# Kernel optimization log

Measured on AMD Instinct MI355X. Metric: run time of the kernel, lower is better.

Reference implementation:

```python
import jax, jax.numpy as jnp
import numpy as np

B, T, H, K = 64, 512, 768, 32


def setup_inputs() -> dict:
    key = jax.random.key(0)
    ks = jax.random.split(key, 6)
    x = jax.random.normal(ks[0], (B, T, H), jnp.float32)
    y = jax.random.randint(ks[1], (B, T), 0, K)
    sequence_lengths = jax.random.randint(ks[2], (B,), 1, T + 1)
    W = jax.random.normal(ks[3], (H, K), jnp.float32) * 0.02
    b = jnp.zeros((K,), jnp.float32)
    transition_params = jax.random.normal(ks[4], (K, K), jnp.float32) * 0.1
    return dict(x=x, y=y, sequence_lengths=sequence_lengths, W=W, b=b,
                transition_params=transition_params)


def _crf_log_norm(pot, lengths, trans):
    # pot: [B,T,K]; forward algorithm with per-example length masking
    alpha0 = pot[:, 0]
    def step(alpha, inp):
        pot_t, t = inp
        new = jax.nn.logsumexp(alpha[:, :, None] + trans[None], axis=1) + pot_t
        keep = (t < lengths)[:, None]
        return jnp.where(keep, new, alpha), None
    xs = (jnp.swapaxes(pot[:, 1:], 0, 1), jnp.arange(1, pot.shape[1]))
    alpha, _ = jax.lax.scan(step, alpha0, xs)
    return jax.nn.logsumexp(alpha, axis=-1)  # [B]


def _crf_sequence_score(pot, y, lengths, trans):
    t_idx = jnp.arange(pot.shape[1])
    mask_u = (t_idx[None, :] < lengths[:, None]).astype(pot.dtype)      # [B,T]
    unary = jnp.take_along_axis(pot, y[..., None], axis=2)[..., 0]      # [B,T]
    unary = jnp.sum(unary * mask_u, axis=1)
    mask_b = (t_idx[None, :-1] < (lengths - 1)[:, None]).astype(pot.dtype)
    binary = trans[y[:, :-1], y[:, 1:]]                                 # [B,T-1]
    binary = jnp.sum(binary * mask_b, axis=1)
    return unary + binary


def _crf_decode(pot, lengths, trans):
    Bb, Tt, Kk = pot.shape
    alpha0 = pot[:, 0]
    ident = jnp.broadcast_to(jnp.arange(Kk), (Bb, Kk))
    def fwd(alpha, inp):
        pot_t, t = inp
        scores = alpha[:, :, None] + trans[None]   # [B,K,K] prev->cur
        bp = jnp.argmax(scores, axis=1)            # [B,K]
        new = jnp.max(scores, axis=1) + pot_t
        keep = (t < lengths)[:, None]
        alpha = jnp.where(keep, new, alpha)
        bp = jnp.where(keep, bp, ident)            # identity past end of seq
        return alpha, bp
    xs = (jnp.swapaxes(pot[:, 1:], 0, 1), jnp.arange(1, Tt))
    alpha, bps = jax.lax.scan(fwd, alpha0, xs)     # bps: [T-1,B,K]
    last = jnp.argmax(alpha, axis=-1)              # [B]
    def back(tag, bp):
        prev = jnp.take_along_axis(bp, tag[:, None], axis=1)[:, 0]
        return prev, prev
    _, prevs = jax.lax.scan(back, last, bps, reverse=True)  # [T-1,B]
    tags = jnp.concatenate([prevs, last[None]], axis=0).T   # [B,T]
    return tags


def reference(x, y, sequence_lengths, W, b, transition_params):
    pot = jnp.einsum('bth,hk->btk', x, W) + b      # dense projection to tag space
    log_likelihood = (_crf_sequence_score(pot, y, sequence_lengths, transition_params)
                      - _crf_log_norm(pot, sequence_lengths, transition_params))
    preds = _crf_decode(pot, sequence_lengths, transition_params)
    mask = (jnp.arange(pot.shape[1])[None, :] < sequence_lengths[:, None]).astype(preds.dtype)
    preds = preds * mask
    return log_likelihood, preds
```

## Files before the change

kernel.cpp:

```cpp
#include <hip/hip_runtime.h>
#include <hip/hip_bf16.h>
#include <stdint.h>


#define TT 512
#define KK 32
#define HH 768
#define NB 64

#define WS_POT 0
#define WS_VA  4198400
#define WS_BP  8396800
#define WS_LOGZ 9445376
#define WS_LAST 9445632

template <int CTRL>
__device__ __forceinline__ float dppx(float x) {
  return __int_as_float(__builtin_amdgcn_update_dpp(
      0, __float_as_int(x), CTRL, 0xF, 0xF, true));
}

__device__ __forceinline__ float xor16f(float x) {
  float d = x, s = x;
  asm volatile("v_permlane16_swap_b32 %0, %1" : "+v"(d), "+v"(s));
  return __uint_as_float(__float_as_uint(d) ^ __float_as_uint(s) ^ __float_as_uint(x));
}
__device__ __forceinline__ float xor32f(float x) {
  float d = x, s = x;
  asm volatile("v_permlane32_swap_b32 %0, %1" : "+v"(d), "+v"(s));
  return __uint_as_float(__float_as_uint(d) ^ __float_as_uint(s) ^ __float_as_uint(x));
}

__device__ __forceinline__ float redmax32(float v) {
  v = fmaxf(v, dppx<0xB1>(v));
  v = fmaxf(v, dppx<0x4E>(v));
  v = fmaxf(v, dppx<0x141>(v));
  v = fmaxf(v, dppx<0x128>(v));
  v = fmaxf(v, xor16f(v));
  return v;
}
__device__ __forceinline__ float redsum32(float v) {
  v += dppx<0xB1>(v);
  v += dppx<0x4E>(v);
  v += dppx<0x141>(v);
  v += dppx<0x128>(v);
  v += xor16f(v);
  return v;
}

__device__ __forceinline__ int gmap(int m) {
  return ((m & 1) ? 1 : 0) ^ ((m & 2) ? 2 : 0) ^ ((m & 4) ? 7 : 0) ^ ((m & 8) ? 8 : 0);
}

#define REPL_TREE(A)                                            \
  A[1] = dppx<0xB1>(A[0]);                                      \
  _Pragma("unroll") for (int p = 0; p < 2; ++p) A[2 + p] = dppx<0x4E>(A[p]);  \
  _Pragma("unroll") for (int p = 0; p < 4; ++p) A[4 + p] = dppx<0x141>(A[p]); \
  _Pragma("unroll") for (int p = 0; p < 8; ++p) A[8 + p] = dppx<0x128>(A[p]);

__global__ __launch_bounds__(256) void gemm_pot(const float* __restrict__ x,
                                                const float* __restrict__ W,
                                                const float* __restrict__ bias,
                                                float* __restrict__ pot) {
  __shared__ float4 xs4[64][16];
  __shared__ float4 wt4[32][16];
  const int tid = threadIdx.x;
  const int row0 = blockIdx.x * 64;
  const int cg = tid & 15;
  const int rg = tid >> 4;
  const int c0 = cg * 2;
  float acc[4][2] = {{0.f, 0.f}, {0.f, 0.f}, {0.f, 0.f}, {0.f, 0.f}};

  for (int h0 = 0; h0 < HH; h0 += 64) {
#pragma unroll
    for (int p = 0; p < 4; ++p) {
      const int fi = tid + p * 256;
      const int r = fi >> 4, s = fi & 15;
      const float4 v = *(const float4*)(&x[(size_t)(row0 + r) * HH + h0 + s * 4]);
      xs4[r][s ^ ((r >> 2) & 3)] = v;
    }
    {
      const int c = tid & 31;
      const int hb = (tid >> 5) * 8;
      float* wf = (float*)(&wt4[0][0]);
#pragma unroll
      for (int i2 = 0; i2 < 8; ++i2) {
        const int hh = hb + i2;
        const int slot = (hh >> 2) ^ ((c >> 1) & 15);
        wf[c * 64 + slot * 4 + (hh & 3)] = W[(size_t)(h0 + hh) * KK + c];
      }
    }
    __syncthreads();
#pragma unroll
    for (int s = 0; s < 16; ++s) {
      float4 xv[4];
#pragma unroll
      for (int i = 0; i < 4; ++i) xv[i] = xs4[rg * 4 + i][s ^ (rg & 3)];
      const float4 wv0 = wt4[c0][s ^ cg];
      const float4 wv1 = wt4[c0 + 1][s ^ cg];
#pragma unroll
      for (int i = 0; i < 4; ++i) {
        acc[i][0] += xv[i].x * wv0.x + xv[i].y * wv0.y + xv[i].z * wv0.z + xv[i].w * wv0.w;
        acc[i][1] += xv[i].x * wv1.x + xv[i].y * wv1.y + xv[i].z * wv1.z + xv[i].w * wv1.w;
      }
    }
    __syncthreads();
  }
#pragma unroll
  for (int i = 0; i < 4; ++i) {
    const int row = row0 + rg * 4 + i;
    float2 o = make_float2(acc[i][0] + bias[c0], acc[i][1] + bias[c0 + 1]);
    *(float2*)(&pot[(size_t)row * KK + c0]) = o;
  }
}

__global__ __launch_bounds__(64) void scan2(const float* __restrict__ pot,
                                            const int* __restrict__ lens,
                                            const float* __restrict__ trans,
                                            float* __restrict__ va,
                                            float* __restrict__ logZ,
                                            int* __restrict__ last) {
  const int lane = threadIdx.x;
  const int k = lane & 31;
  const int jh = lane >> 5;
  const bool is_lse = (blockIdx.x < 64);
  const int b = is_lse ? blockIdx.x : blockIdx.x - 64;
  const int len = lens[b];
  const float* pp = pot + (size_t)b * (TT * KK) + k;

  if (is_lse) {
    float etrx[16];
#pragma unroll
    for (int m = 0; m < 16; ++m)
      etrx[m] = __expf(trans[((k ^ gmap(m) ^ (jh << 4)) << 5) + k]);
    const float a0 = pp[0];
    const float M0 = redmax32(a0);
    float a = __expf(a0 - M0);
    float alog = M0;
    float ep[8], en[8];
#pragma unroll
    for (int i = 0; i < 8; ++i) ep[i] = __expf(pp[(size_t)(1 + i) * KK]);
    for (int tb = 1; tb < len; tb += 8) {
#pragma unroll
      for (int i = 0; i < 8; ++i) en[i] = pp[(size_t)(tb + 8 + i) * KK];
#pragma unroll
      for (int i = 0; i < 8; ++i) {
        const int t = tb + i;
        if (t >= len) break;
        float A[16];
        const float u16 = xor16f(a);
        A[0] = jh ? u16 : a;
        REPL_TREE(A)
        float d0 = 0.f, d1 = 0.f, d2 = 0.f, d3 = 0.f;
#pragma unroll
        for (int p = 0; p < 4; ++p) {
          d0 += A[4 * p + 0] * etrx[4 * p + 0];
          d1 += A[4 * p + 1] * etrx[4 * p + 1];
          d2 += A[4 * p + 2] * etrx[4 * p + 2];
          d3 += A[4 * p + 3] * etrx[4 * p + 3];
        }
        float part = (d0 + d1) + (d2 + d3);
        a = (part + xor32f(part)) * ep[i];
        if ((t & 7) == 0) {
          const float mx = redmax32(a);
          alog += __logf(mx);
          a *= __builtin_amdgcn_rcpf(mx);
        }
      }
#pragma unroll
      for (int i = 0; i < 8; ++i) ep[i] = __expf(en[i]);
    }
    const float ssum = redsum32(a);
    if (lane == 0) logZ[b] = alog + __logf(ssum);
  } else {
    float trx[16];
#pragma unroll
    for (int m = 0; m < 16; ++m)
      trx[m] = trans[((k ^ gmap(m) ^ (jh << 4)) << 5) + k];
    float a = pp[0];
    float* vap = va + (size_t)b * (TT * KK) + k;
    if (lane < 32) vap[0] = a;
    float pb[8], pn[8];
#pragma unroll
    for (int i = 0; i < 8; ++i) pb[i] = pp[(size_t)(1 + i) * KK];
    for (int tb = 1; tb < len; tb += 8) {
#pragma unroll
      for (int i = 0; i < 8; ++i) pn[i] = pp[(size_t)(tb + 8 + i) * KK];
#pragma unroll
      for (int i = 0; i < 8; ++i) {
        const int t = tb + i;
        if (t >= len) break;
        float A[16];
        const float u16 = xor16f(a);
        A[0] = jh ? u16 : a;
        REPL_TREE(A)
        float s_[16];
#pragma unroll
        for (int m = 0; m < 16; ++m) s_[m] = A[m] + trx[m];
        const float m0 = fmaxf(fmaxf(s_[0], s_[1]), fmaxf(s_[2], s_[3]));
        const float m1 = fmaxf(fmaxf(s_[4], s_[5]), fmaxf(s_[6], s_[7]));
        const float m2 = fmaxf(fmaxf(s_[8], s_[9]), fmaxf(s_[10], s_[11]));
        const float m3 = fmaxf(fmaxf(s_[12], s_[13]), fmaxf(s_[14], s_[15]));
        const float part = fmaxf(fmaxf(m0, m1), fmaxf(m2, m3));
        a = fmaxf(part, xor32f(part)) + pb[i];
        if (lane < 32) vap[(size_t)t * KK] = a;
      }
#pragma unroll
      for (int i = 0; i < 8; ++i) pb[i] = pn[i];
    }
    float v = a;
    int idx = k;
#pragma unroll
    for (int mm = 16; mm >= 1; mm >>= 1) {
      const float vo = __shfl_xor(v, mm, 32);
      const int io = __shfl_xor(idx, mm, 32);
      if (vo > v || (vo == v && io < idx)) { v = vo; idx = io; }
    }
    if (lane == 0) last[b] = idx;
  }
}

__global__ __launch_bounds__(256) void bp_extract(const float* __restrict__ va,
                                                  const float* __restrict__ trans,
                                                  unsigned char* __restrict__ bp) {
  const int b = blockIdx.x >> 3;
  const int tbase = (blockIdx.x & 7) * 64;
  const int k = threadIdx.x & 31;
  const int ts = threadIdx.x >> 5;
  float tr[32];
#pragma unroll
  for (int j = 0; j < 32; ++j) tr[j] = trans[j * KK + k];
#pragma unroll
  for (int it = 0; it < 8; ++it) {
    const int t = tbase + it * 8 + ts;
    if (t < 1) continue;
    const float* row = va + ((size_t)b * TT + (t - 1)) * KK;
    float best = row[0] + tr[0];
    int bi = 0;
#pragma unroll
    for (int j = 1; j < 32; ++j) {
      const float s = row[j] + tr[j];
      if (s > best) { best = s; bi = j; }
    }
    bp[((size_t)b * TT + t) * KK + k] = (unsigned char)bi;
  }
}

__global__ __launch_bounds__(256) void backtrace_kernel(
    const unsigned char* __restrict__ bp, const int* __restrict__ lens,
    const int* __restrict__ last, const float* __restrict__ pot,
    const int* __restrict__ y, const float* __restrict__ trans,
    const float* __restrict__ logZ, float* __restrict__ out) {
  __shared__ unsigned char Ls[32736];
  __shared__ unsigned char sA[512], sB[512];
  __shared__ float red[256];
  const int b = blockIdx.x, tid = threadIdx.x;
  const int len = lens[b];

  for (int i = tid; i < TT * KK; i += 256) {
    const int t = i >> 5, k = i & 31;
    Ls[i] = (t >= 1 && t < len) ? bp[((size_t)b * TT + t) * KK + k] : (unsigned char)k;
  }
  __syncthreads();

  int off_prev = 0, cnt = 512;
  for (int l = 1; l <= 9; ++l) {
    const int off = 32 * (1024 - (1024 >> l));
    const int n = cnt >> 1;
    for (int i = tid; i < n * 32; i += 256) {
      const int m = i >> 5, k = i & 31;
      const int inner = Ls[off_prev + (2 * m + 1) * 32 + k];
      Ls[off + i] = Ls[off_prev + (2 * m) * 32 + inner];
    }
    __syncthreads();
    off_prev = off;
    cnt = n;
  }

  if (tid == 0) sA[0] = (unsigned char)last[b];
  __syncthreads();

  unsigned char* cur = sA;
  unsigned char* nxt = sB;
  int c2 = 1;
  for (int l = 9; l >= 1; --l) {
    const int offm = 32 * (1024 - (1024 >> (l - 1)));
    for (int i = tid; i < c2; i += 256) {
      const unsigned char s = cur[i];
      nxt[2 * i + 1] = s;
      nxt[2 * i] = Ls[offm + (2 * i + 1) * 32 + s];
    }
    __syncthreads();
    unsigned char* tmp = cur; cur = nxt; nxt = tmp;
    c2 <<= 1;
  }

  for (int t = tid; t < TT; t += 256)
    out[NB + (size_t)b * TT + t] = (t < len) ? (float)cur[t] : 0.f;

  float acc = 0.f;
  for (int t = tid; t < TT; t += 256) {
    const int yt = y[b * TT + t];
    if (t < len) acc += pot[((size_t)b * TT + t) * KK + yt];
    if (t < len - 1) acc += trans[yt * KK + y[b * TT + t + 1]];
  }
  red[tid] = acc;
  __syncthreads();
  for (int s = 128; s >= 1; s >>= 1) {
    if (tid < s) red[tid] += red[tid + s];
    __syncthreads();
  }
  if (tid == 0) out[b] = red[0] - logZ[b];
}

extern "C" void kernel_launch(void* const* d_in, const int* in_sizes, int n_in,
                              void* d_out, int out_size, void* d_ws, size_t ws_size,
                              hipStream_t stream) {
  const float* x = (const float*)d_in[0];
  const int* y = (const int*)d_in[1];
  const int* lens = (const int*)d_in[2];
  const float* W = (const float*)d_in[3];
  const float* bias = (const float*)d_in[4];
  const float* trans = (const float*)d_in[5];
  float* out = (float*)d_out;
  char* ws = (char*)d_ws;
  float* pot = (float*)(ws + WS_POT);
  float* va = (float*)(ws + WS_VA);
  unsigned char* bp = (unsigned char*)(ws + WS_BP);
  float* logZ = (float*)(ws + WS_LOGZ);
  int* last = (int*)(ws + WS_LAST);

  gemm_pot<<<512, 256, 0, stream>>>(x, W, bias, pot);
  scan2<<<128, 64, 0, stream>>>(pot, lens, trans, va, logZ, last);
  bp_extract<<<512, 256, 0, stream>>>(va, trans, bp);
  backtrace_kernel<<<64, 256, 0, stream>>>(bp, lens, last, pot, y, trans, logZ, out);
}
```

Measured before the change: 152.6 us.

## Parallelize CRF forward and Viterbi scans via chunked semiring matrix products

Replaces the serial per-sequence scan kernel with a three-phase parallel scan. Phase A builds 32x32 transfer matrices (sum-product for the log-normalizer, max-plus for Viterbi) for each 8-step chunk. Phase B scans the 64 chunk matrices per sequence to produce chunk-boundary alphas, logZ and the last tag. Phase C replays each chunk in parallel from its boundary alpha to fill the per-step Viterbi scores. This exposes far more parallelism than 128 single-wave blocks walking 512 steps, at the cost of much more total arithmetic, about 34 MB of extra workspace traffic and two extra launches.

```diff
diff --git a/kernel.cpp b/kernel.cpp
--- a/kernel.cpp
+++ b/kernel.cpp
@@ -8,18 +8,21 @@
 #define HH 768
 #define NB 64
 
-#define WS_POT 0
-#define WS_VA  4198400
-#define WS_BP  8396800
+#define WS_POT  0
+#define WS_VA   4198400
+#define WS_BP   8396800
 #define WS_LOGZ 9445376
 #define WS_LAST 9445632
+#define WS_MLSE 9445888
+#define WS_SLSE 26223104
+#define WS_MVIT 26239488
+#define WS_VB   43016704
 
 template <int CTRL>
 __device__ __forceinline__ float dppx(float x) {
   return __int_as_float(__builtin_amdgcn_update_dpp(
       0, __float_as_int(x), CTRL, 0xF, 0xF, true));
 }
-
 __device__ __forceinline__ float xor16f(float x) {
   float d = x, s = x;
   asm volatile("v_permlane16_swap_b32 %0, %1" : "+v"(d), "+v"(s));
@@ -30,6 +33,21 @@
   asm volatile("v_permlane32_swap_b32 %0, %1" : "+v"(d), "+v"(s));
   return __uint_as_float(__float_as_uint(d) ^ __float_as_uint(s) ^ __float_as_uint(x));
 }
+
+__device__ __forceinline__ int gmap(int m) {
+  return ((m & 1) ? 1 : 0) ^ ((m & 2) ? 2 : 0) ^ ((m & 4) ? 7 : 0) ^ ((m & 8) ? 8 : 0);
+}
+__device__ __forceinline__ int g5(int m) { return gmap(m & 15) ^ ((m & 16) ? 16 : 0); }
+
+#define REPL_TREE(A)                                            \
+  A[1] = dppx<0xB1>(A[0]);                                      \
+  _Pragma("unroll") for (int p = 0; p < 2; ++p) A[2 + p] = dppx<0x4E>(A[p]);  \
+  _Pragma("unroll") for (int p = 0; p < 4; ++p) A[4 + p] = dppx<0x141>(A[p]); \
+  _Pragma("unroll") for (int p = 0; p < 8; ++p) A[8 + p] = dppx<0x128>(A[p]);
+
+#define REPL_TREE32(A)                                          \
+  REPL_TREE(A)                                                  \
+  _Pragma("unroll") for (int p = 0; p < 16; ++p) A[16 + p] = xor16f(A[p]);
 
 __device__ __forceinline__ float redmax32(float v) {
   v = fmaxf(v, dppx<0xB1>(v));
@@ -47,16 +65,6 @@
   v += xor16f(v);
   return v;
 }
-
-__device__ __forceinline__ int gmap(int m) {
-  return ((m & 1) ? 1 : 0) ^ ((m & 2) ? 2 : 0) ^ ((m & 4) ? 7 : 0) ^ ((m & 8) ? 8 : 0);
-}
-
-#define REPL_TREE(A)                                            \
-  A[1] = dppx<0xB1>(A[0]);                                      \
-  _Pragma("unroll") for (int p = 0; p < 2; ++p) A[2 + p] = dppx<0x4E>(A[p]);  \
-  _Pragma("unroll") for (int p = 0; p < 4; ++p) A[4 + p] = dppx<0x141>(A[p]); \
-  _Pragma("unroll") for (int p = 0; p < 8; ++p) A[8 + p] = dppx<0x128>(A[p]);
 
 __global__ __launch_bounds__(256) void gemm_pot(const float* __restrict__ x,
                                                 const float* __restrict__ W,
@@ -114,109 +122,281 @@
   }
 }
 
-__global__ __launch_bounds__(64) void scan2(const float* __restrict__ pot,
-                                            const int* __restrict__ lens,
-                                            const float* __restrict__ trans,
-                                            float* __restrict__ va,
-                                            float* __restrict__ logZ,
-                                            int* __restrict__ last) {
-  const int lane = threadIdx.x;
+__global__ __launch_bounds__(256) void phaseA(const float* __restrict__ pot,
+                                              const int* __restrict__ lens,
+                                              const float* __restrict__ trans,
+                                              float* __restrict__ maps_lse,
+                                              float* __restrict__ scale_lse,
+                                              float* __restrict__ maps_vit) {
+  __shared__ float E[1024];
+  const int tid = threadIdx.x;
+  const bool is_lse = (blockIdx.x < 1024);
+  const int blk = is_lse ? blockIdx.x : blockIdx.x - 1024;
+  const int b = blk >> 4;
+  const int c = (blk & 15) * 4 + (tid >> 6);
+  const int lane = tid & 63;
+  const int j = lane >> 1, h = lane & 1;
+
+#pragma unroll
+  for (int q = 0; q < 4; ++q) {
+    const float v = trans[tid + q * 256];
+    E[tid + q * 256] = is_lse ? __expf(v) : v;
+  }
+  __syncthreads();
+
+  const int len = lens[b];
+  const int t0 = 8 * c + 1;
+  const int t1 = min(8 * c + 8, len - 1);
+  const size_t id = (size_t)b * 64 + c;
+  float* outp = (is_lse ? maps_lse : maps_vit) + id * 1024 + (j * 32 + 16 * h);
+  float M[16];
+
+  if (t0 > t1) {
+#pragma unroll
+    for (int i = 0; i < 16; ++i)
+      M[i] = is_lse ? ((16 * h + i) == j ? 1.f : 0.f)
+                    : ((16 * h + i) == j ? 0.f : -1e30f);
+    if (is_lse && lane == 0) scale_lse[id] = 0.f;
+  } else {
+    const float4* Eb = (const float4*)E;
+    {
+      const float4* p4 = (const float4*)(pot + ((size_t)b * TT + t0) * KK + 16 * h);
+      float4 d0 = p4[0], d1 = p4[1], d2 = p4[2], d3 = p4[3];
+      float dv[16] = {d0.x, d0.y, d0.z, d0.w, d1.x, d1.y, d1.z, d1.w,
+                      d2.x, d2.y, d2.z, d2.w, d3.x, d3.y, d3.z, d3.w};
+      if (is_lse) {
+#pragma unroll
+        for (int i = 0; i < 16; ++i) dv[i] = __expf(dv[i]);
+      }
+#pragma unroll
+      for (int i = 0; i < 16; ++i) {
+        const float e = E[j * 32 + 16 * h + i];
+        M[i] = is_lse ? e * dv[i] : e + dv[i];
+      }
+    }
+    for (int t = t0 + 1; t <= t1; ++t) {
+      const float4* p4 = (const float4*)(pot + ((size_t)b * TT + t) * KK + 16 * h);
+      float4 d0 = p4[0], d1 = p4[1], d2 = p4[2], d3 = p4[3];
+      float dv[16] = {d0.x, d0.y, d0.z, d0.w, d1.x, d1.y, d1.z, d1.w,
+                      d2.x, d2.y, d2.z, d2.w, d3.x, d3.y, d3.z, d3.w};
+      float Mp[16];
+#pragma unroll
+      for (int i = 0; i < 16; ++i) Mp[i] = dppx<0xB1>(M[i]);
+      float acc[16];
+#pragma unroll
+      for (int i = 0; i < 16; ++i) acc[i] = is_lse ? 0.f : -1e30f;
+
+#define ROWOP(mval, ridx)                                                     \
+      {                                                                       \
+        const float4 e0 = Eb[(ridx) * 8 + 4 * h + 0];                         \
+        const float4 e1 = Eb[(ridx) * 8 + 4 * h + 1];                         \
+        const float4 e2 = Eb[(ridx) * 8 + 4 * h + 2];                         \
+        const float4 e3 = Eb[(ridx) * 8 + 4 * h + 3];                         \
+        if (is_lse) {                                                         \
+          acc[0] += (mval) * e0.x;  acc[1] += (mval) * e0.y;                  \
+          acc[2] += (mval) * e0.z;  acc[3] += (mval) * e0.w;                  \
+          acc[4] += (mval) * e1.x;  acc[5] += (mval) * e1.y;                  \
+          acc[6] += (mval) * e1.z;  acc[7] += (mval) * e1.w;                  \
+          acc[8] += (mval) * e2.x;  acc[9] += (mval) * e2.y;                  \
+          acc[10] += (mval) * e2.z; acc[11] += (mval) * e2.w;                 \
+          acc[12] += (mval) * e3.x; acc[13] += (mval) * e3.y;                 \
+          acc[14] += (mval) * e3.z; acc[15] += (mval) * e3.w;                 \
+        } else {                                                              \
+          acc[0] = fmaxf(acc[0], (mval) + e0.x);  acc[1] = fmaxf(acc[1], (mval) + e0.y);  \
+          acc[2] = fmaxf(acc[2], (mval) + e0.z);  acc[3] = fmaxf(acc[3], (mval) + e0.w);  \
+          acc[4] = fmaxf(acc[4], (mval) + e1.x);  acc[5] = fmaxf(acc[5], (mval) + e1.y);  \
+          acc[6] = fmaxf(acc[6], (mval) + e1.z);  acc[7] = fmaxf(acc[7], (mval) + e1.w);  \
+          acc[8] = fmaxf(acc[8], (mval) + e2.x);  acc[9] = fmaxf(acc[9], (mval) + e2.y);  \
+          acc[10] = fmaxf(acc[10], (mval) + e2.z); acc[11] = fmaxf(acc[11], (mval) + e2.w); \
+          acc[12] = fmaxf(acc[12], (mval) + e3.x); acc[13] = fmaxf(acc[13], (mval) + e3.y); \
+          acc[14] = fmaxf(acc[14], (mval) + e3.z); acc[15] = fmaxf(acc[15], (mval) + e3.w); \
+        }                                                                     \
+      }
+
+#pragma unroll
+      for (int i2 = 0; i2 < 16; ++i2) ROWOP(M[i2], 16 * h + i2)
+#pragma unroll
+      for (int i2 = 0; i2 < 16; ++i2) ROWOP(Mp[i2], 16 * (1 - h) + i2)
+#undef ROWOP
+      if (is_lse) {
+#pragma unroll
+        for (int i = 0; i < 16; ++i) M[i] = acc[i] * __expf(dv[i]);
+      } else {
+#pragma unroll
+        for (int i = 0; i < 16; ++i) M[i] = acc[i] + dv[i];
+      }
+    }
+    if (is_lse) {
+      float mx = M[0];
+#pragma unroll
+      for (int i = 1; i < 16; ++i) mx = fmaxf(mx, M[i]);
+      mx = fmaxf(mx, dppx<0xB1>(mx));
+      mx = fmaxf(mx, dppx<0x4E>(mx));
+      mx = fmaxf(mx, dppx<0x141>(mx));
+      mx = fmaxf(mx, dppx<0x128>(mx));
+      mx = fmaxf(mx, xor16f(mx));
+      mx = fmaxf(mx, xor32f(mx));
+      const float inv = __builtin_amdgcn_rcpf(mx);
+#pragma unroll
+      for (int i = 0; i < 16; ++i) M[i] *= inv;
+      if (lane == 0) scale_lse[id] = __logf(mx);
+    }
+  }
+  float4* o4 = (float4*)outp;
+#pragma unroll
+  for (int q = 0; q < 4; ++q)
+    o4[q] = make_float4(M[4 * q], M[4 * q + 1], M[4 * q + 2], M[4 * q + 3]);
+}
+
+__global__ __launch_bounds__(256) void phaseB(const float* __restrict__ pot,
+                                              const float* __restrict__ maps_lse,
+                                              const float* __restrict__ scale_lse,
+                                              const float* __restrict__ maps_vit,
+                                              float* __restrict__ vb,
+                                              float* __restrict__ logZ,
+                                              int* __restrict__ last) {
+  __shared__ float mbuf[2][8192];
+  __shared__ float sscale;
+  const int tid = threadIdx.x;
+  const bool is_lse = (blockIdx.x < 64);
+  const int b = is_lse ? blockIdx.x : blockIdx.x - 64;
+  const float* maps = (is_lse ? maps_lse : maps_vit) + (size_t)b * 65536;
+
+  {
+    const float4* src = (const float4*)maps;
+    for (int q = tid; q < 2048; q += 256) ((float4*)mbuf[0])[q] = src[q];
+  }
+  if (is_lse && tid == 64) {
+    float s = 0.f;
+#pragma unroll 8
+    for (int cc = 0; cc < 64; ++cc) s += scale_lse[b * 64 + cc];
+    sscale = s;
+  }
+  __syncthreads();
+
+  const int k = tid;
+  float aown = 0.f, alog = 0.f;
+  int addr[32];
+  if (tid < 32) {
+#pragma unroll
+    for (int m = 0; m < 32; ++m) addr[m] = ((k ^ g5(m)) << 5) + k;
+    const float a0 = pot[(size_t)b * (TT * KK) + k];
+    if (is_lse) {
+      const float m0 = redmax32(a0);
+      aown = __expf(a0 - m0);
+      alog = m0;
+    } else {
+      aown = a0;
+    }
+  }
+
+  for (int r = 0; r < 8; ++r) {
+    if (r < 7 && tid >= 64) {
+      const float4* src = (const float4*)(maps + (size_t)(r + 1) * 8192);
+      float4* dst = (float4*)mbuf[(r + 1) & 1];
+      for (int q = tid - 64; q < 2048; q += 192) dst[q] = src[q];
+    }
+    if (tid < 32) {
+      const float* mb0 = mbuf[r & 1];
+#pragma unroll 1
+      for (int m2 = 0; m2 < 8; ++m2) {
+        const float* mb = mb0 + m2 * 1024;
+        const int cc = r * 8 + m2;
+        if (!is_lse) vb[((size_t)b * 64 + cc) * 32 + k] = aown;
+        float mv[32];
+#pragma unroll
+        for (int m = 0; m < 32; ++m) mv[m] = mb[addr[m]];
+        float A[32];
+        A[0] = aown;
+        REPL_TREE32(A)
+        if (is_lse) {
+          float mxA = A[0];
+#pragma unroll
+          for (int m = 1; m < 32; ++m) mxA = fmaxf(mxA, A[m]);
+          float s0 = 0.f, s1 = 0.f, s2 = 0.f, s3 = 0.f;
+#pragma unroll
+          for (int p = 0; p < 8; ++p) {
+            s0 += A[4 * p + 0] * mv[4 * p + 0];
+            s1 += A[4 * p + 1] * mv[4 * p + 1];
+            s2 += A[4 * p + 2] * mv[4 * p + 2];
+            s3 += A[4 * p + 3] * mv[4 * p + 3];
+          }
+          aown = ((s0 + s1) + (s2 + s3)) * __builtin_amdgcn_rcpf(mxA);
+          alog += __logf(mxA);
+        } else {
+          float s0 = -1e30f, s1 = -1e30f, s2 = -1e30f, s3 = -1e30f;
+#pragma unroll
+          for (int p = 0; p < 8; ++p) {
+            s0 = fmaxf(s0, A[4 * p + 0] + mv[4 * p + 0]);
+            s1 = fmaxf(s1, A[4 * p + 1] + mv[4 * p + 1]);
+            s2 = fmaxf(s2, A[4 * p + 2] + mv[4 * p + 2]);
+            s3 = fmaxf(s3, A[4 * p + 3] + mv[4 * p + 3]);
+          }
+          aown = fmaxf(fmaxf(s0, s1), fmaxf(s2, s3));
+        }
+      }
+    }
+    __syncthreads();
+  }
+  if (tid < 32) {
+    if (is_lse) {
+      const float ssum = redsum32(aown);
+      if (k == 0) logZ[b] = alog + __logf(ssum) + sscale;
+    } else {
+      float v = aown;
+      int idx = k;
+#pragma unroll
+      for (int mm = 16; mm >= 1; mm >>= 1) {
+        const float vo = __shfl_xor(v, mm, 32);
+        const int io = __shfl_xor(idx, mm, 32);
+        if (vo > v || (vo == v && io < idx)) { v = vo; idx = io; }
+      }
+      if (k == 0) last[b] = idx;
+    }
+  }
+}
+
+__global__ __launch_bounds__(256) void phaseC(const float* __restrict__ pot,
+                                              const int* __restrict__ lens,
+                                              const float* __restrict__ trans,
+                                              const float* __restrict__ vb,
+                                              float* __restrict__ va) {
+  const int tid = threadIdx.x;
+  const int lane = tid & 63;
   const int k = lane & 31;
   const int jh = lane >> 5;
-  const bool is_lse = (blockIdx.x < 64);
-  const int b = is_lse ? blockIdx.x : blockIdx.x - 64;
+  const int id = blockIdx.x * 4 + (tid >> 6);
+  const int b = id >> 6, c = id & 63;
   const int len = lens[b];
+  float trx[16];
+#pragma unroll
+  for (int m = 0; m < 16; ++m)
+    trx[m] = trans[((k ^ gmap(m) ^ (jh << 4)) << 5) + k];
   const float* pp = pot + (size_t)b * (TT * KK) + k;
-
-  if (is_lse) {
-    float etrx[16];
-#pragma unroll
-    for (int m = 0; m < 16; ++m)
-      etrx[m] = __expf(trans[((k ^ gmap(m) ^ (jh << 4)) << 5) + k]);
-    const float a0 = pp[0];
-    const float M0 = redmax32(a0);
-    float a = __expf(a0 - M0);
-    float alog = M0;
-    float ep[8], en[8];
-#pragma unroll
-    for (int i = 0; i < 8; ++i) ep[i] = __expf(pp[(size_t)(1 + i) * KK]);
-    for (int tb = 1; tb < len; tb += 8) {
-#pragma unroll
-      for (int i = 0; i < 8; ++i) en[i] = pp[(size_t)(tb + 8 + i) * KK];
-#pragma unroll
-      for (int i = 0; i < 8; ++i) {
-        const int t = tb + i;
-        if (t >= len) break;
-        float A[16];
-        const float u16 = xor16f(a);
-        A[0] = jh ? u16 : a;
-        REPL_TREE(A)
-        float d0 = 0.f, d1 = 0.f, d2 = 0.f, d3 = 0.f;
-#pragma unroll
-        for (int p = 0; p < 4; ++p) {
-          d0 += A[4 * p + 0] * etrx[4 * p + 0];
-          d1 += A[4 * p + 1] * etrx[4 * p + 1];
-          d2 += A[4 * p + 2] * etrx[4 * p + 2];
-          d3 += A[4 * p + 3] * etrx[4 * p + 3];
-        }
-        float part = (d0 + d1) + (d2 + d3);
-        a = (part + xor32f(part)) * ep[i];
-        if ((t & 7) == 0) {
-          const float mx = redmax32(a);
-          alog += __logf(mx);
-          a *= __builtin_amdgcn_rcpf(mx);
-        }
-      }
-#pragma unroll
-      for (int i = 0; i < 8; ++i) ep[i] = __expf(en[i]);
-    }
-    const float ssum = redsum32(a);
-    if (lane == 0) logZ[b] = alog + __logf(ssum);
-  } else {
-    float trx[16];
-#pragma unroll
-    for (int m = 0; m < 16; ++m)
-      trx[m] = trans[((k ^ gmap(m) ^ (jh << 4)) << 5) + k];
-    float a = pp[0];
-    float* vap = va + (size_t)b * (TT * KK) + k;
-    if (lane < 32) vap[0] = a;
-    float pb[8], pn[8];
-#pragma unroll
-    for (int i = 0; i < 8; ++i) pb[i] = pp[(size_t)(1 + i) * KK];
-    for (int tb = 1; tb < len; tb += 8) {
-#pragma unroll
-      for (int i = 0; i < 8; ++i) pn[i] = pp[(size_t)(tb + 8 + i) * KK];
-#pragma unroll
-      for (int i = 0; i < 8; ++i) {
-        const int t = tb + i;
-        if (t >= len) break;
-        float A[16];
-        const float u16 = xor16f(a);
-        A[0] = jh ? u16 : a;
-        REPL_TREE(A)
-        float s_[16];
-#pragma unroll
-        for (int m = 0; m < 16; ++m) s_[m] = A[m] + trx[m];
-        const float m0 = fmaxf(fmaxf(s_[0], s_[1]), fmaxf(s_[2], s_[3]));
-        const float m1 = fmaxf(fmaxf(s_[4], s_[5]), fmaxf(s_[6], s_[7]));
-        const float m2 = fmaxf(fmaxf(s_[8], s_[9]), fmaxf(s_[10], s_[11]));
-        const float m3 = fmaxf(fmaxf(s_[12], s_[13]), fmaxf(s_[14], s_[15]));
-        const float part = fmaxf(fmaxf(m0, m1), fmaxf(m2, m3));
-        a = fmaxf(part, xor32f(part)) + pb[i];
-        if (lane < 32) vap[(size_t)t * KK] = a;
-      }
-#pragma unroll
-      for (int i = 0; i < 8; ++i) pb[i] = pn[i];
-    }
-    float v = a;
-    int idx = k;
-#pragma unroll
-    for (int mm = 16; mm >= 1; mm >>= 1) {
-      const float vo = __shfl_xor(v, mm, 32);
-      const int io = __shfl_xor(idx, mm, 32);
-      if (vo > v || (vo == v && io < idx)) { v = vo; idx = io; }
-    }
-    if (lane == 0) last[b] = idx;
+  float a = vb[(size_t)id * 32 + k];
+  float* vap = va + ((size_t)b * TT + 8 * c) * KK + k;
+  if (lane < 32) vap[0] = a;
+  float pb[7];
+#pragma unroll
+  for (int i = 0; i < 7; ++i) pb[i] = pp[(size_t)(8 * c + 1 + i) * KK];
+#pragma unroll
+  for (int s = 0; s < 7; ++s) {
+    const int t = 8 * c + 1 + s;
+    float A[16];
+    const float u16 = xor16f(a);
+    A[0] = jh ? u16 : a;
+    REPL_TREE(A)
+    float s_[16];
+#pragma unroll
+    for (int m = 0; m < 16; ++m) s_[m] = A[m] + trx[m];
+    const float m0 = fmaxf(fmaxf(s_[0], s_[1]), fmaxf(s_[2], s_[3]));
+    const float m1 = fmaxf(fmaxf(s_[4], s_[5]), fmaxf(s_[6], s_[7]));
+    const float m2 = fmaxf(fmaxf(s_[8], s_[9]), fmaxf(s_[10], s_[11]));
+    const float m3 = fmaxf(fmaxf(s_[12], s_[13]), fmaxf(s_[14], s_[15]));
+    const float part = fmaxf(fmaxf(m0, m1), fmaxf(m2, m3));
+    const float anew = fmaxf(part, xor32f(part)) + pb[s];
+    a = (t < len) ? anew : a;
+    if (lane < 32) vap[(size_t)(s + 1) * KK] = a;
   }
 }
 
@@ -329,9 +509,15 @@
   unsigned char* bp = (unsigned char*)(ws + WS_BP);
   float* logZ = (float*)(ws + WS_LOGZ);
   int* last = (int*)(ws + WS_LAST);
+  float* maps_lse = (float*)(ws + WS_MLSE);
+  float* s_lse = (float*)(ws + WS_SLSE);
+  float* maps_vit = (float*)(ws + WS_MVIT);
+  float* vbp = (float*)(ws + WS_VB);
 
   gemm_pot<<<512, 256, 0, stream>>>(x, W, bias, pot);
-  scan2<<<128, 64, 0, stream>>>(pot, lens, trans, va, logZ, last);
+  phaseA<<<2048, 256, 0, stream>>>(pot, lens, trans, maps_lse, s_lse, maps_vit);
+  phaseB<<<128, 256, 0, stream>>>(pot, maps_lse, s_lse, maps_vit, vbp, logZ, last);
+  phaseC<<<1024, 256, 0, stream>>>(pot, lens, trans, vbp, va);
   bp_extract<<<512, 256, 0, stream>>>(va, trans, bp);
   backtrace_kernel<<<64, 256, 0, stream>>>(bp, lens, last, pot, y, trans, logZ, out);
 }
```

Result: slower. 524.3 us (+243.5%).
